# Performance work log

Measured on AMD Instinct MI355X. Metric: run time of the kernel, lower is better.

Reference implementation:

```python
import jax, jax.numpy as jnp
import numpy as np

N = 100000
E = 3200000
T = 8
F = 64


def _temporal_conv(x, src, dst, time_index, W, b):
    # time-bucketed segmented scatter-add: segment id = dst*T + t
    seg = dst * T + time_index                      # [E]
    msgs = x[src]                                   # [E, F] gather (x_j)
    agg = jax.ops.segment_sum(msgs, seg, num_segments=N * T)  # [N*T, F]
    cat = agg.reshape(N, T * x.shape[-1])           # concat over t blocks: [N, T*F]
    return jax.nn.relu(cat @ W + b)                 # temporal_lin + relu


def setup_inputs() -> dict:
    key = jax.random.key(0)
    ks = jax.random.split(key, 10)
    x = jax.random.normal(ks[0], (N, F), dtype=jnp.float32)
    edge_index = jax.random.randint(ks[1], (2, E), 0, N, dtype=jnp.int64)
    time_index = jax.random.randint(ks[2], (E,), 0, T, dtype=jnp.int64)
    s1 = 1.0 / np.sqrt(F * T)
    W1 = jax.random.uniform(ks[3], (F * T, 64), jnp.float32, -s1, s1)
    b1 = jax.random.uniform(ks[4], (64,), jnp.float32, -s1, s1)
    s2 = 1.0 / np.sqrt(64 * T)
    W2 = jax.random.uniform(ks[5], (64 * T, 64), jnp.float32, -s2, s2)
    b2 = jax.random.uniform(ks[6], (64,), jnp.float32, -s2, s2)
    s3 = 1.0 / np.sqrt(64)
    Wssl = jax.random.uniform(ks[7], (64, F), jnp.float32, -s3, s3)
    bssl = jax.random.uniform(ks[8], (F,), jnp.float32, -s3, s3)
    return {"x": x, "edge_index": edge_index, "time_index": time_index,
            "W1": W1, "b1": b1, "W2": W2, "b2": b2, "Wssl": Wssl, "bssl": bssl}


def reference(x, edge_index, time_index, W1, b1, W2, b2, Wssl, bssl):
    src, dst = edge_index[0], edge_index[1]  # flow source_to_target
    h = _temporal_conv(x, src, dst, time_index, W1, b1)
    h = jax.nn.relu(h)                        # outer relu in TemporalSSTGNN.forward
    h = _temporal_conv(h, src, dst, time_index, W2, b2)
    ssl = h @ Wssl + bssl                     # self_supervised_linear
    return (h, ssl)
```

## Files before the change

kernel.cpp:

```cpp
#include <hip/hip_runtime.h>
#include <hip/hip_bf16.h>

#define N_NODES 100000
#define N_EDGES 3200000
#define NB 391
#define NBP 400
#define CAP 9216
#define PCAP 20480
#define ZNODE N_NODES
#define NTILES 6250
#define AROW 520

typedef __attribute__((ext_vector_type(8))) short short8;
typedef __attribute__((ext_vector_type(4))) float floatx4;

__device__ __forceinline__ float bf2f(unsigned short u) {
    unsigned int x = ((unsigned int)u) << 16;
    return __builtin_bit_cast(float, x);
}
__device__ __forceinline__ unsigned short f2bf(float f) {
    unsigned int u = __builtin_bit_cast(unsigned int, f);
    unsigned int r = (u + 0x7FFFu + ((u >> 16) & 1u)) >> 16;
    return (unsigned short)r;
}


__global__ __launch_bounds__(1024) void k_bscatter(const int* __restrict__ ei,
                                                   const int* __restrict__ ti,
                                                   int* __restrict__ cursor,
                                                   unsigned int* __restrict__ words) {
    __shared__ int h[NBP];
    __shared__ int bb[NBP];
    int tid = threadIdx.x;
    if (tid < NBP) h[tid] = 0;
    __syncthreads();
    int base = blockIdx.x * 4096;
    int breg[4], ofs[4];
    unsigned wreg[4];
#pragma unroll
    for (int i = 0; i < 4; ++i) {
        int e = base + i * 1024 + tid;
        bool v = e < N_EDGES;
        int dst = v ? ei[N_EDGES + e] : 0;
        int src = v ? ei[e] : 0;
        int tt  = v ? ti[e] : 0;
        int b = dst >> 8;
        breg[i] = v ? b : -1;
        wreg[i] = ((unsigned)src << 11) | ((unsigned)(dst & 255) << 3) | (unsigned)tt;
        ofs[i] = v ? atomicAdd(&h[b], 1) : 0;
    }
    __syncthreads();
    if (tid < NB) {
        int c = h[tid];
        bb[tid] = c ? atomicAdd(&cursor[tid], c) : 0;
    }
    __syncthreads();
#pragma unroll
    for (int i = 0; i < 4; ++i)
        if (breg[i] >= 0) {
            int b = breg[i];
            words[b * CAP + bb[b] + ofs[i]] = wreg[i];
        }
}

__global__ __launch_bounds__(1024) void k_lsort(const int* __restrict__ cursor,
                                                const unsigned int* __restrict__ words,
                                                int2* __restrict__ node_pm,
                                                int* __restrict__ gid_pad) {
    __shared__ int h[2048];
    __shared__ int ps[1024];
    __shared__ int nb[256];
    __shared__ int s_ml[256];
    int tid = threadIdx.x;
    int b = blockIdx.x;
    int rb = b * CAP, re = rb + cursor[b];
    h[tid] = 0; h[tid + 1024] = 0;
    __syncthreads();
    unsigned wreg[9];
    int ofs[9];
#pragma unroll
    for (int i = 0; i < 9; ++i) {
        int e = rb + i * 1024 + tid;
        bool v = e < re;
        unsigned w = v ? words[e] : 0u;
        wreg[i] = w;
        ofs[i] = v ? atomicAdd(&h[w & 2047u], 1) : -1;
    }
    __syncthreads();
    int sz = 0;
    if (tid < 256) {
        int m = 0;
#pragma unroll
        for (int t = 0; t < 8; ++t) { int c = h[tid * 8 + t]; m = c > m ? c : m; }
        m = (m + 3) & ~3;
        if (m < 8) m = 8;
        s_ml[tid] = m;
        sz = m * 8;
    }
    ps[tid] = sz;
    __syncthreads();
    for (int off = 1; off < 1024; off <<= 1) {
        int t = (tid >= off) ? ps[tid - off] : 0;
        __syncthreads();
        ps[tid] += t;
        __syncthreads();
    }
    if (tid < 256) nb[tid] = ps[tid] - sz;
    __syncthreads();
    int bsz = ps[1023];
    int pbase = b * PCAP;
    for (int s = tid; s < bsz; s += 1024) gid_pad[pbase + s] = ZNODE;
    int gn = b * 256 + tid;
    if (tid < 256 && gn < N_NODES) node_pm[gn] = (int2){pbase + nb[tid], s_ml[tid]};
    __syncthreads();
#pragma unroll
    for (int i = 0; i < 9; ++i)
        if (ofs[i] >= 0) {
            unsigned w = wreg[i];
            int ls = (int)(w & 2047u);
            int nd = ls >> 3, t = ls & 7;
            gid_pad[pbase + nb[nd] + t * s_ml[nd] + ofs[i]] = (int)(w >> 11);
        }
}


__global__ void k_cvt(const float* __restrict__ x, unsigned short* __restrict__ xb,
                      unsigned short* __restrict__ h1b,
                      const float* __restrict__ W1, const float* __restrict__ W2,
                      const float* __restrict__ Wssl,
                      unsigned short* __restrict__ Wf1, unsigned short* __restrict__ Wf2,
                      unsigned short* __restrict__ Wsf) {
    int i = blockIdx.x * 256 + threadIdx.x;
    if (i < N_NODES * 64) xb[i] = f2bf(x[i]);
    if (i < 64) {
        xb[(size_t)ZNODE * 64 + i] = 0;
        h1b[(size_t)ZNODE * 64 + i] = 0;
    }
    if (i < 512 * 64) {
        int k = i >> 6, o = i & 63;
        int c = o >> 4, m = o & 15;
        int ks = k >> 5, q = (k >> 3) & 3, j = k & 7;
        int pos = (((c * 16 + ks) * 64) + (m + 16 * q)) * 8 + j;
        Wf1[pos] = f2bf(W1[i]);
        Wf2[pos] = f2bf(W2[i]);
    }
    if (i < 64 * 64) {
        int k = i >> 6, o = i & 63;
        int c = o >> 4, m = o & 15;
        int ks = k >> 5, q = (k >> 3) & 3, j = k & 7;
        int pos = (((c * 2 + ks) * 64) + (m + 16 * q)) * 8 + j;
        Wsf[pos] = f2bf(Wssl[i]);
    }
}


__device__ __forceinline__ void accum8(float* a, uint4 p) {
    a[0] += __builtin_bit_cast(float, p.x << 16);
    a[1] += __builtin_bit_cast(float, p.x & 0xFFFF0000u);
    a[2] += __builtin_bit_cast(float, p.y << 16);
    a[3] += __builtin_bit_cast(float, p.y & 0xFFFF0000u);
    a[4] += __builtin_bit_cast(float, p.z << 16);
    a[5] += __builtin_bit_cast(float, p.z & 0xFFFF0000u);
    a[6] += __builtin_bit_cast(float, p.w << 16);
    a[7] += __builtin_bit_cast(float, p.w & 0xFFFF0000u);
}

__global__ __launch_bounds__(512) void k_fused(const int2* __restrict__ node_pm,
                                               const int* __restrict__ gid_pad,
                                               const unsigned short* __restrict__ xb,
                                               const unsigned short* __restrict__ Wf,
                                               const float* __restrict__ bias,
                                               unsigned short* __restrict__ out_bf,
                                               float* __restrict__ out_f32) {
    __shared__ __align__(16) unsigned short Atile[32 * AROW];
    int tid = threadIdx.x;
    int wave = tid >> 6, lane = tid & 63;
    int node_base = blockIdx.x * 32;
    int tl = lane >> 3, fo = lane & 7;
    const uint4* xs = (const uint4*)xb;

    int2 pm[4];
#pragma unroll
    for (int i = 0; i < 4; ++i) pm[i] = node_pm[node_base + wave * 4 + i];

#pragma unroll
    for (int i = 0; i < 4; ++i) {
        int nl = wave * 4 + i;
        int pb = __builtin_amdgcn_readfirstlane(pm[i].x);
        int ml = __builtin_amdgcn_readfirstlane(pm[i].y);
        const int* gp = gid_pad + pb + tl * ml;
        float acc[8] = {0.f, 0.f, 0.f, 0.f, 0.f, 0.f, 0.f, 0.f};
        int k = 0;
#pragma unroll 1
        for (; k + 8 <= ml; k += 8) {
            int4 ga = *(const int4*)(gp + k);
            int4 gb = *(const int4*)(gp + k + 4);
            uint4 p0 = xs[((unsigned)ga.x << 3) + fo];
            uint4 p1 = xs[((unsigned)ga.y << 3) + fo];
            uint4 p2 = xs[((unsigned)ga.z << 3) + fo];
            uint4 p3 = xs[((unsigned)ga.w << 3) + fo];
            uint4 p4 = xs[((unsigned)gb.x << 3) + fo];
            uint4 p5 = xs[((unsigned)gb.y << 3) + fo];
            uint4 p6 = xs[((unsigned)gb.z << 3) + fo];
            uint4 p7 = xs[((unsigned)gb.w << 3) + fo];
            accum8(acc, p0); accum8(acc, p1); accum8(acc, p2); accum8(acc, p3);
            accum8(acc, p4); accum8(acc, p5); accum8(acc, p6); accum8(acc, p7);
        }
        if (k < ml) {
            int4 ga = *(const int4*)(gp + k);
            uint4 p0 = xs[((unsigned)ga.x << 3) + fo];
            uint4 p1 = xs[((unsigned)ga.y << 3) + fo];
            uint4 p2 = xs[((unsigned)ga.z << 3) + fo];
            uint4 p3 = xs[((unsigned)ga.w << 3) + fo];
            accum8(acc, p0); accum8(acc, p1); accum8(acc, p2); accum8(acc, p3);
        }
        unsigned r0, r1, r2, r3;
        asm("v_cvt_pk_bf16_f32 %0, %1, %2" : "=v"(r0) : "v"(acc[0]), "v"(acc[1]));
        asm("v_cvt_pk_bf16_f32 %0, %1, %2" : "=v"(r1) : "v"(acc[2]), "v"(acc[3]));
        asm("v_cvt_pk_bf16_f32 %0, %1, %2" : "=v"(r2) : "v"(acc[4]), "v"(acc[5]));
        asm("v_cvt_pk_bf16_f32 %0, %1, %2" : "=v"(r3) : "v"(acc[6]), "v"(acc[7]));
        uint4 st;
        st.x = r0; st.y = r1; st.z = r2; st.w = r3;
        *(uint4*)(&Atile[nl * AROW + tl * 64 + fo * 8]) = st;
    }
    __syncthreads();

    int nt = wave >> 2, c = wave & 3;
    int m = lane & 15, q = lane >> 4;
    floatx4 acc = (floatx4){0.f, 0.f, 0.f, 0.f};
    const short8* wf8 = (const short8*)Wf;
    const unsigned short* abase = &Atile[(nt * 16 + m) * AROW + q * 8];
#pragma unroll
    for (int ks = 0; ks < 16; ++ks) {
        short8 a = *(const short8*)(abase + ks * 32);
        short8 b = wf8[(c * 16 + ks) * 64 + lane];
        acc = __builtin_amdgcn_mfma_f32_16x16x32_bf16(a, b, acc, 0, 0, 0);
    }
    float bb = bias[c * 16 + m];
    int node0 = node_base + nt * 16;
#pragma unroll
    for (int i = 0; i < 4; ++i) {
        float v = acc[i] + bb;
        v = v > 0.f ? v : 0.f;
        int node = node0 + q * 4 + i;
        size_t idx = (size_t)node * 64 + c * 16 + m;
        if (out_bf)  out_bf[idx] = f2bf(v);
        if (out_f32) out_f32[idx] = v;
    }
}


__global__ __launch_bounds__(256) void k_sslm(const unsigned short* __restrict__ h2b,
                                              const unsigned short* __restrict__ Wsf,
                                              const float* __restrict__ bssl,
                                              float* __restrict__ out) {
    int wave = threadIdx.x >> 6, lane = threadIdx.x & 63;
    int tile = blockIdx.x * 4 + wave;
    if (tile >= NTILES) return;
    int m = lane & 15, q = lane >> 4;
    const unsigned short* arow = h2b + ((size_t)(tile * 16 + m)) * 64 + q * 8;
    floatx4 acc[4];
    for (int c = 0; c < 4; ++c) acc[c] = (floatx4){0.f, 0.f, 0.f, 0.f};
    const short8* wf8 = (const short8*)Wsf;
#pragma unroll
    for (int ks = 0; ks < 2; ++ks) {
        short8 a = *(const short8*)(arow + ks * 32);
#pragma unroll
        for (int c = 0; c < 4; ++c) {
            short8 b = wf8[(c * 2 + ks) * 64 + lane];
            acc[c] = __builtin_amdgcn_mfma_f32_16x16x32_bf16(a, b, acc[c], 0, 0, 0);
        }
    }
    int node0 = tile * 16;
#pragma unroll
    for (int c = 0; c < 4; ++c) {
        float bb = bssl[c * 16 + m];
#pragma unroll
        for (int i = 0; i < 4; ++i) {
            int node = node0 + q * 4 + i;
            out[(size_t)node * 64 + c * 16 + m] = acc[c][i] + bb;
        }
    }
}


extern "C" void kernel_launch(void* const* d_in, const int* in_sizes, int n_in,
                              void* d_out, int out_size, void* d_ws, size_t ws_size,
                              hipStream_t stream) {
    const float* x    = (const float*)d_in[0];
    const int*   ei   = (const int*)d_in[1];
    const int*   ti   = (const int*)d_in[2];
    const float* W1   = (const float*)d_in[3];
    const float* b1   = (const float*)d_in[4];
    const float* W2   = (const float*)d_in[5];
    const float* b2   = (const float*)d_in[6];
    const float* Wssl = (const float*)d_in[7];
    const float* bssl = (const float*)d_in[8];
    float* out = (float*)d_out;

    char* w = (char*)d_ws;
    auto alloc = [&](size_t bytes) -> char* {
        char* p = w;
        w += (bytes + 255) & ~(size_t)255;
        return p;
    };
    int* cursor   = (int*)alloc((size_t)NBP * 4);
    unsigned int* words = (unsigned int*)alloc((size_t)NB * CAP * 4);
    int2* node_pm = (int2*)alloc((size_t)N_NODES * 8);
    int* gid_pad  = (int*)alloc((size_t)NB * PCAP * 4);
    unsigned short* xb  = (unsigned short*)alloc((size_t)(N_NODES + 1) * 64 * 2);
    unsigned short* h1b = (unsigned short*)alloc((size_t)(N_NODES + 1) * 64 * 2);
    unsigned short* h2b = (unsigned short*)alloc((size_t)N_NODES * 64 * 2);
    unsigned short* Wf1 = (unsigned short*)alloc((size_t)512 * 64 * 2);
    unsigned short* Wf2 = (unsigned short*)alloc((size_t)512 * 64 * 2);
    unsigned short* Wsf = (unsigned short*)alloc((size_t)64 * 64 * 2);

    hipMemsetAsync(cursor, 0, (size_t)NBP * 4, stream);
    k_bscatter<<<(N_EDGES + 4095) / 4096, 1024, 0, stream>>>(ei, ti, cursor, words);
    k_lsort<<<NB, 1024, 0, stream>>>(cursor, words, node_pm, gid_pad);
    k_cvt<<<(N_NODES * 64 + 255) / 256, 256, 0, stream>>>(x, xb, h1b, W1, W2, Wssl,
                                                          Wf1, Wf2, Wsf);

    k_fused<<<N_NODES / 32, 512, 0, stream>>>(node_pm, gid_pad, xb, Wf1, b1, h1b, nullptr);
    k_fused<<<N_NODES / 32, 512, 0, stream>>>(node_pm, gid_pad, h1b, Wf2, b2, h2b, out);

    k_sslm<<<(NTILES + 3) / 4, 256, 0, stream>>>(h2b, Wsf, bssl, out + (size_t)N_NODES * 64);
}
```

Before: 323.7 us.

## Fuse conversion into scatter, SSL linear into second conv, restructure gather loop

Folds the bf16 conversion of x and the weights into the bucket-scatter kernel, with a vectorized packed convert, which drops one launch. Fuses the self-supervised 64x64 linear into the second fused conv kernel through shared memory, removing the h2 bf16 round trip and the k_sslm launch. The local sort prefix scan is replaced by wave shuffles. The gather loop now prefetches index lists for all four nodes and processes nodes in pairs with packed float2 accumulation to raise memory-level parallelism. The risks are higher register pressure in the fused kernel and a longer serialized tail in the scatter kernel.

```diff
diff --git a/kernel.cpp b/kernel.cpp
--- a/kernel.cpp
+++ b/kernel.cpp
@@ -8,27 +8,32 @@
 #define CAP 9216
 #define PCAP 20480
 #define ZNODE N_NODES
-#define NTILES 6250
 #define AROW 520
+#define HROW 72
 
 typedef __attribute__((ext_vector_type(8))) short short8;
 typedef __attribute__((ext_vector_type(4))) float floatx4;
-
-__device__ __forceinline__ float bf2f(unsigned short u) {
-    unsigned int x = ((unsigned int)u) << 16;
-    return __builtin_bit_cast(float, x);
-}
+typedef __attribute__((ext_vector_type(2))) float f32x2;
+
 __device__ __forceinline__ unsigned short f2bf(float f) {
     unsigned int u = __builtin_bit_cast(unsigned int, f);
     unsigned int r = (u + 0x7FFFu + ((u >> 16) & 1u)) >> 16;
     return (unsigned short)r;
 }
 
-
 __global__ __launch_bounds__(1024) void k_bscatter(const int* __restrict__ ei,
                                                    const int* __restrict__ ti,
                                                    int* __restrict__ cursor,
-                                                   unsigned int* __restrict__ words) {
+                                                   unsigned int* __restrict__ words,
+                                                   const float* __restrict__ x,
+                                                   unsigned short* __restrict__ xb,
+                                                   unsigned short* __restrict__ h1b,
+                                                   const float* __restrict__ W1,
+                                                   const float* __restrict__ W2,
+                                                   const float* __restrict__ Wssl,
+                                                   unsigned short* __restrict__ Wf1,
+                                                   unsigned short* __restrict__ Wf2,
+                                                   unsigned short* __restrict__ Wsf) {
     __shared__ int h[NBP];
     __shared__ int bb[NBP];
     int tid = threadIdx.x;
@@ -61,6 +66,39 @@
             int b = breg[i];
             words[b * CAP + bb[b] + ofs[i]] = wreg[i];
         }
+
+    int gtid = blockIdx.x * 1024 + tid;
+    size_t xo = (size_t)gtid * 8;
+    if (xo < (size_t)N_NODES * 64) {
+        float4 f0 = *(const float4*)(x + xo);
+        float4 f1 = *(const float4*)(x + xo + 4);
+        unsigned r0, r1, r2, r3;
+        asm("v_cvt_pk_bf16_f32 %0, %1, %2" : "=v"(r0) : "v"(f0.x), "v"(f0.y));
+        asm("v_cvt_pk_bf16_f32 %0, %1, %2" : "=v"(r1) : "v"(f0.z), "v"(f0.w));
+        asm("v_cvt_pk_bf16_f32 %0, %1, %2" : "=v"(r2) : "v"(f1.x), "v"(f1.y));
+        asm("v_cvt_pk_bf16_f32 %0, %1, %2" : "=v"(r3) : "v"(f1.z), "v"(f1.w));
+        uint4 st; st.x = r0; st.y = r1; st.z = r2; st.w = r3;
+        *(uint4*)(xb + xo) = st;
+    }
+    if (gtid < 64) {
+        xb[(size_t)ZNODE * 64 + gtid] = 0;
+        h1b[(size_t)ZNODE * 64 + gtid] = 0;
+    }
+    if (gtid < 512 * 64) {
+        int k = gtid >> 6, o = gtid & 63;
+        int c = o >> 4, m = o & 15;
+        int ks = k >> 5, q = (k >> 3) & 3, j = k & 7;
+        int pos = (((c * 16 + ks) * 64) + (m + 16 * q)) * 8 + j;
+        Wf1[pos] = f2bf(W1[gtid]);
+        Wf2[pos] = f2bf(W2[gtid]);
+    }
+    if (gtid < 64 * 64) {
+        int k = gtid >> 6, o = gtid & 63;
+        int c = o >> 4, m = o & 15;
+        int ks = k >> 5, q = (k >> 3) & 3, j = k & 7;
+        int pos = (((c * 2 + ks) * 64) + (m + 16 * q)) * 8 + j;
+        Wsf[pos] = f2bf(Wssl[gtid]);
+    }
 }
 
 __global__ __launch_bounds__(1024) void k_lsort(const int* __restrict__ cursor,
@@ -68,9 +106,9 @@
                                                 int2* __restrict__ node_pm,
                                                 int* __restrict__ gid_pad) {
     __shared__ int h[2048];
-    __shared__ int ps[1024];
     __shared__ int nb[256];
     __shared__ int s_ml[256];
+    __shared__ int wsum[4];
     int tid = threadIdx.x;
     int b = blockIdx.x;
     int rb = b * CAP, re = rb + cursor[b];
@@ -97,17 +135,21 @@
         s_ml[tid] = m;
         sz = m * 8;
     }
-    ps[tid] = sz;
-    __syncthreads();
-    for (int off = 1; off < 1024; off <<= 1) {
-        int t = (tid >= off) ? ps[tid - off] : 0;
-        __syncthreads();
-        ps[tid] += t;
-        __syncthreads();
-    }
-    if (tid < 256) nb[tid] = ps[tid] - sz;
-    __syncthreads();
-    int bsz = ps[1023];
+    int lane = tid & 63, wv = tid >> 6;
+    int inc = sz;
+#pragma unroll
+    for (int off = 1; off < 64; off <<= 1) {
+        int t = __shfl_up(inc, off, 64);
+        if (lane >= off) inc += t;
+    }
+    if (tid < 256 && lane == 63) wsum[wv] = inc;
+    __syncthreads();
+    int bsz = wsum[0] + wsum[1] + wsum[2] + wsum[3];
+    if (tid < 256) {
+        int basec = 0;
+        for (int w = 0; w < wv; ++w) basec += wsum[w];
+        nb[tid] = basec + inc - sz;
+    }
     int pbase = b * PCAP;
     for (int s = tid; s < bsz; s += 1024) gid_pad[pbase + s] = ZNODE;
     int gn = b * 256 + tid;
@@ -124,45 +166,16 @@
 }
 
 
-__global__ void k_cvt(const float* __restrict__ x, unsigned short* __restrict__ xb,
-                      unsigned short* __restrict__ h1b,
-                      const float* __restrict__ W1, const float* __restrict__ W2,
-                      const float* __restrict__ Wssl,
-                      unsigned short* __restrict__ Wf1, unsigned short* __restrict__ Wf2,
-                      unsigned short* __restrict__ Wsf) {
-    int i = blockIdx.x * 256 + threadIdx.x;
-    if (i < N_NODES * 64) xb[i] = f2bf(x[i]);
-    if (i < 64) {
-        xb[(size_t)ZNODE * 64 + i] = 0;
-        h1b[(size_t)ZNODE * 64 + i] = 0;
-    }
-    if (i < 512 * 64) {
-        int k = i >> 6, o = i & 63;
-        int c = o >> 4, m = o & 15;
-        int ks = k >> 5, q = (k >> 3) & 3, j = k & 7;
-        int pos = (((c * 16 + ks) * 64) + (m + 16 * q)) * 8 + j;
-        Wf1[pos] = f2bf(W1[i]);
-        Wf2[pos] = f2bf(W2[i]);
-    }
-    if (i < 64 * 64) {
-        int k = i >> 6, o = i & 63;
-        int c = o >> 4, m = o & 15;
-        int ks = k >> 5, q = (k >> 3) & 3, j = k & 7;
-        int pos = (((c * 2 + ks) * 64) + (m + 16 * q)) * 8 + j;
-        Wsf[pos] = f2bf(Wssl[i]);
-    }
-}
-
-
-__device__ __forceinline__ void accum8(float* a, uint4 p) {
-    a[0] += __builtin_bit_cast(float, p.x << 16);
-    a[1] += __builtin_bit_cast(float, p.x & 0xFFFF0000u);
-    a[2] += __builtin_bit_cast(float, p.y << 16);
-    a[3] += __builtin_bit_cast(float, p.y & 0xFFFF0000u);
-    a[4] += __builtin_bit_cast(float, p.z << 16);
-    a[5] += __builtin_bit_cast(float, p.z & 0xFFFF0000u);
-    a[6] += __builtin_bit_cast(float, p.w << 16);
-    a[7] += __builtin_bit_cast(float, p.w & 0xFFFF0000u);
+__device__ __forceinline__ void accumP(f32x2* a, uint4 p) {
+    uint2 u;
+    u.x = p.x << 16; u.y = p.x & 0xFFFF0000u;
+    a[0] += __builtin_bit_cast(f32x2, u);
+    u.x = p.y << 16; u.y = p.y & 0xFFFF0000u;
+    a[1] += __builtin_bit_cast(f32x2, u);
+    u.x = p.z << 16; u.y = p.z & 0xFFFF0000u;
+    a[2] += __builtin_bit_cast(f32x2, u);
+    u.x = p.w << 16; u.y = p.w & 0xFFFF0000u;
+    a[3] += __builtin_bit_cast(f32x2, u);
 }
 
 __global__ __launch_bounds__(512) void k_fused(const int2* __restrict__ node_pm,
@@ -170,8 +183,11 @@
                                                const unsigned short* __restrict__ xb,
                                                const unsigned short* __restrict__ Wf,
                                                const float* __restrict__ bias,
+                                               const unsigned short* __restrict__ Wsf,
+                                               const float* __restrict__ bssl,
                                                unsigned short* __restrict__ out_bf,
-                                               float* __restrict__ out_f32) {
+                                               float* __restrict__ out_f32,
+                                               float* __restrict__ ssl_out) {
     __shared__ __align__(16) unsigned short Atile[32 * AROW];
     int tid = threadIdx.x;
     int wave = tid >> 6, lane = tid & 63;
@@ -183,45 +199,77 @@
 #pragma unroll
     for (int i = 0; i < 4; ++i) pm[i] = node_pm[node_base + wave * 4 + i];
 
+    int pb[4], ml[4];
+    const int* gp[4];
 #pragma unroll
     for (int i = 0; i < 4; ++i) {
-        int nl = wave * 4 + i;
-        int pb = __builtin_amdgcn_readfirstlane(pm[i].x);
-        int ml = __builtin_amdgcn_readfirstlane(pm[i].y);
-        const int* gp = gid_pad + pb + tl * ml;
-        float acc[8] = {0.f, 0.f, 0.f, 0.f, 0.f, 0.f, 0.f, 0.f};
-        int k = 0;
+        pb[i] = __builtin_amdgcn_readfirstlane(pm[i].x);
+        ml[i] = __builtin_amdgcn_readfirstlane(pm[i].y);
+        gp[i] = gid_pad + pb[i] + tl * ml[i];
+    }
+    int4 ga[4], gb[4];
+#pragma unroll
+    for (int i = 0; i < 4; ++i) {
+        ga[i] = *(const int4*)(gp[i]);
+        gb[i] = *(const int4*)(gp[i] + 4);
+    }
+
+#pragma unroll
+    for (int pr = 0; pr < 2; ++pr) {
+        int i0 = pr * 2, i1 = i0 + 1;
+        uint4 p0 = xs[((unsigned)ga[i0].x << 3) + fo];
+        uint4 p1 = xs[((unsigned)ga[i0].y << 3) + fo];
+        uint4 p2 = xs[((unsigned)ga[i0].z << 3) + fo];
+        uint4 p3 = xs[((unsigned)ga[i0].w << 3) + fo];
+        uint4 p4 = xs[((unsigned)gb[i0].x << 3) + fo];
+        uint4 p5 = xs[((unsigned)gb[i0].y << 3) + fo];
+        uint4 p6 = xs[((unsigned)gb[i0].z << 3) + fo];
+        uint4 p7 = xs[((unsigned)gb[i0].w << 3) + fo];
+        uint4 q0 = xs[((unsigned)ga[i1].x << 3) + fo];
+        uint4 q1 = xs[((unsigned)ga[i1].y << 3) + fo];
+        uint4 q2 = xs[((unsigned)ga[i1].z << 3) + fo];
+        uint4 q3 = xs[((unsigned)ga[i1].w << 3) + fo];
+        uint4 q4 = xs[((unsigned)gb[i1].x << 3) + fo];
+        uint4 q5 = xs[((unsigned)gb[i1].y << 3) + fo];
+        uint4 q6 = xs[((unsigned)gb[i1].z << 3) + fo];
+        uint4 q7 = xs[((unsigned)gb[i1].w << 3) + fo];
+        f32x2 a0[4] = {{0.f,0.f},{0.f,0.f},{0.f,0.f},{0.f,0.f}};
+        f32x2 a1[4] = {{0.f,0.f},{0.f,0.f},{0.f,0.f},{0.f,0.f}};
+        accumP(a0, p0); accumP(a0, p1); accumP(a0, p2); accumP(a0, p3);
+        accumP(a0, p4); accumP(a0, p5); accumP(a0, p6); accumP(a0, p7);
+        accumP(a1, q0); accumP(a1, q1); accumP(a1, q2); accumP(a1, q3);
+        accumP(a1, q4); accumP(a1, q5); accumP(a1, q6); accumP(a1, q7);
 #pragma unroll 1
-        for (; k + 8 <= ml; k += 8) {
-            int4 ga = *(const int4*)(gp + k);
-            int4 gb = *(const int4*)(gp + k + 4);
-            uint4 p0 = xs[((unsigned)ga.x << 3) + fo];
-            uint4 p1 = xs[((unsigned)ga.y << 3) + fo];
-            uint4 p2 = xs[((unsigned)ga.z << 3) + fo];
-            uint4 p3 = xs[((unsigned)ga.w << 3) + fo];
-            uint4 p4 = xs[((unsigned)gb.x << 3) + fo];
-            uint4 p5 = xs[((unsigned)gb.y << 3) + fo];
-            uint4 p6 = xs[((unsigned)gb.z << 3) + fo];
-            uint4 p7 = xs[((unsigned)gb.w << 3) + fo];
-            accum8(acc, p0); accum8(acc, p1); accum8(acc, p2); accum8(acc, p3);
-            accum8(acc, p4); accum8(acc, p5); accum8(acc, p6); accum8(acc, p7);
-        }
-        if (k < ml) {
-            int4 ga = *(const int4*)(gp + k);
-            uint4 p0 = xs[((unsigned)ga.x << 3) + fo];
-            uint4 p1 = xs[((unsigned)ga.y << 3) + fo];
-            uint4 p2 = xs[((unsigned)ga.z << 3) + fo];
-            uint4 p3 = xs[((unsigned)ga.w << 3) + fo];
-            accum8(acc, p0); accum8(acc, p1); accum8(acc, p2); accum8(acc, p3);
+        for (int k = 8; k < ml[i0]; k += 4) {
+            int4 g = *(const int4*)(gp[i0] + k);
+            uint4 t0 = xs[((unsigned)g.x << 3) + fo];
+            uint4 t1 = xs[((unsigned)g.y << 3) + fo];
+            uint4 t2 = xs[((unsigned)g.z << 3) + fo];
+            uint4 t3 = xs[((unsigned)g.w << 3) + fo];
+            accumP(a0, t0); accumP(a0, t1); accumP(a0, t2); accumP(a0, t3);
+        }
+#pragma unroll 1
+        for (int k = 8; k < ml[i1]; k += 4) {
+            int4 g = *(const int4*)(gp[i1] + k);
+            uint4 t0 = xs[((unsigned)g.x << 3) + fo];
+            uint4 t1 = xs[((unsigned)g.y << 3) + fo];
+            uint4 t2 = xs[((unsigned)g.z << 3) + fo];
+            uint4 t3 = xs[((unsigned)g.w << 3) + fo];
+            accumP(a1, t0); accumP(a1, t1); accumP(a1, t2); accumP(a1, t3);
         }
         unsigned r0, r1, r2, r3;
-        asm("v_cvt_pk_bf16_f32 %0, %1, %2" : "=v"(r0) : "v"(acc[0]), "v"(acc[1]));
-        asm("v_cvt_pk_bf16_f32 %0, %1, %2" : "=v"(r1) : "v"(acc[2]), "v"(acc[3]));
-        asm("v_cvt_pk_bf16_f32 %0, %1, %2" : "=v"(r2) : "v"(acc[4]), "v"(acc[5]));
-        asm("v_cvt_pk_bf16_f32 %0, %1, %2" : "=v"(r3) : "v"(acc[6]), "v"(acc[7]));
-        uint4 st;
+        asm("v_cvt_pk_bf16_f32 %0, %1, %2" : "=v"(r0) : "v"(a0[0].x), "v"(a0[0].y));
+        asm("v_cvt_pk_bf16_f32 %0, %1, %2" : "=v"(r1) : "v"(a0[1].x), "v"(a0[1].y));
+        asm("v_cvt_pk_bf16_f32 %0, %1, %2" : "=v"(r2) : "v"(a0[2].x), "v"(a0[2].y));
+        asm("v_cvt_pk_bf16_f32 %0, %1, %2" : "=v"(r3) : "v"(a0[3].x), "v"(a0[3].y));
+        uint4 st; st.x = r0; st.y = r1; st.z = r2; st.w = r3;
+        *(uint4*)(&Atile[(wave * 4 + i0) * AROW + tl * 64 + fo * 8]) = st;
+        asm("v_cvt_pk_bf16_f32 %0, %1, %2" : "=v"(r0) : "v"(a1[0].x), "v"(a1[0].y));
+        asm("v_cvt_pk_bf16_f32 %0, %1, %2" : "=v"(r1) : "v"(a1[1].x), "v"(a1[1].y));
+        asm("v_cvt_pk_bf16_f32 %0, %1, %2" : "=v"(r2) : "v"(a1[2].x), "v"(a1[2].y));
+        asm("v_cvt_pk_bf16_f32 %0, %1, %2" : "=v"(r3) : "v"(a1[3].x), "v"(a1[3].y));
         st.x = r0; st.y = r1; st.z = r2; st.w = r3;
-        *(uint4*)(&Atile[nl * AROW + tl * 64 + fo * 8]) = st;
+        *(uint4*)(&Atile[(wave * 4 + i1) * AROW + tl * 64 + fo * 8]) = st;
     }
     __syncthreads();
 
@@ -238,47 +286,42 @@
     }
     float bb = bias[c * 16 + m];
     int node0 = node_base + nt * 16;
+    float vv[4];
 #pragma unroll
     for (int i = 0; i < 4; ++i) {
         float v = acc[i] + bb;
-        v = v > 0.f ? v : 0.f;
+        vv[i] = v > 0.f ? v : 0.f;
         int node = node0 + q * 4 + i;
         size_t idx = (size_t)node * 64 + c * 16 + m;
-        if (out_bf)  out_bf[idx] = f2bf(v);
-        if (out_f32) out_f32[idx] = v;
-    }
-}
-
-
-__global__ __launch_bounds__(256) void k_sslm(const unsigned short* __restrict__ h2b,
-                                              const unsigned short* __restrict__ Wsf,
-                                              const float* __restrict__ bssl,
-                                              float* __restrict__ out) {
-    int wave = threadIdx.x >> 6, lane = threadIdx.x & 63;
-    int tile = blockIdx.x * 4 + wave;
-    if (tile >= NTILES) return;
-    int m = lane & 15, q = lane >> 4;
-    const unsigned short* arow = h2b + ((size_t)(tile * 16 + m)) * 64 + q * 8;
-    floatx4 acc[4];
-    for (int c = 0; c < 4; ++c) acc[c] = (floatx4){0.f, 0.f, 0.f, 0.f};
-    const short8* wf8 = (const short8*)Wsf;
-#pragma unroll
-    for (int ks = 0; ks < 2; ++ks) {
-        short8 a = *(const short8*)(arow + ks * 32);
-#pragma unroll
-        for (int c = 0; c < 4; ++c) {
-            short8 b = wf8[(c * 2 + ks) * 64 + lane];
-            acc[c] = __builtin_amdgcn_mfma_f32_16x16x32_bf16(a, b, acc[c], 0, 0, 0);
-        }
-    }
-    int node0 = tile * 16;
-#pragma unroll
-    for (int c = 0; c < 4; ++c) {
-        float bb = bssl[c * 16 + m];
+        if (out_bf)  out_bf[idx] = f2bf(vv[i]);
+        if (out_f32) out_f32[idx] = vv[i];
+    }
+
+    if (ssl_out) {
+        __syncthreads();
+        unsigned short* Ht = Atile;
 #pragma unroll
         for (int i = 0; i < 4; ++i) {
-            int node = node0 + q * 4 + i;
-            out[(size_t)node * 64 + c * 16 + m] = acc[c][i] + bb;
+            int nl = nt * 16 + q * 4 + i;
+            Ht[nl * HROW + c * 16 + m] = f2bf(vv[i]);
+        }
+        __syncthreads();
+        int nt2 = wave >> 2, c2 = wave & 3;
+        floatx4 sacc = (floatx4){0.f, 0.f, 0.f, 0.f};
+        const short8* sw8 = (const short8*)Wsf;
+        const unsigned short* sab = &Ht[(nt2 * 16 + m) * HROW + q * 8];
+#pragma unroll
+        for (int ks = 0; ks < 2; ++ks) {
+            short8 a = *(const short8*)(sab + ks * 32);
+            short8 b = sw8[(c2 * 2 + ks) * 64 + lane];
+            sacc = __builtin_amdgcn_mfma_f32_16x16x32_bf16(a, b, sacc, 0, 0, 0);
+        }
+        float sb = bssl[c2 * 16 + m];
+        int n0 = node_base + nt2 * 16;
+#pragma unroll
+        for (int i = 0; i < 4; ++i) {
+            int node = n0 + q * 4 + i;
+            ssl_out[(size_t)node * 64 + c2 * 16 + m] = sacc[i] + sb;
         }
     }
 }
@@ -310,19 +353,19 @@
     int* gid_pad  = (int*)alloc((size_t)NB * PCAP * 4);
     unsigned short* xb  = (unsigned short*)alloc((size_t)(N_NODES + 1) * 64 * 2);
     unsigned short* h1b = (unsigned short*)alloc((size_t)(N_NODES + 1) * 64 * 2);
-    unsigned short* h2b = (unsigned short*)alloc((size_t)N_NODES * 64 * 2);
     unsigned short* Wf1 = (unsigned short*)alloc((size_t)512 * 64 * 2);
     unsigned short* Wf2 = (unsigned short*)alloc((size_t)512 * 64 * 2);
     unsigned short* Wsf = (unsigned short*)alloc((size_t)64 * 64 * 2);
 
     hipMemsetAsync(cursor, 0, (size_t)NBP * 4, stream);
-    k_bscatter<<<(N_EDGES + 4095) / 4096, 1024, 0, stream>>>(ei, ti, cursor, words);
+    k_bscatter<<<(N_EDGES + 4095) / 4096, 1024, 0, stream>>>(ei, ti, cursor, words,
+                                                             x, xb, h1b, W1, W2, Wssl,
+                                                             Wf1, Wf2, Wsf);
     k_lsort<<<NB, 1024, 0, stream>>>(cursor, words, node_pm, gid_pad);
-    k_cvt<<<(N_NODES * 64 + 255) / 256, 256, 0, stream>>>(x, xb, h1b, W1, W2, Wssl,
-                                                          Wf1, Wf2, Wsf);
-
-    k_fused<<<N_NODES / 32, 512, 0, stream>>>(node_pm, gid_pad, xb, Wf1, b1, h1b, nullptr);
-    k_fused<<<N_NODES / 32, 512, 0, stream>>>(node_pm, gid_pad, h1b, Wf2, b2, h2b, out);
-
-    k_sslm<<<(NTILES + 3) / 4, 256, 0, stream>>>(h2b, Wsf, bssl, out + (size_t)N_NODES * 64);
-}
+
+    k_fused<<<N_NODES / 32, 512, 0, stream>>>(node_pm, gid_pad, xb, Wf1, b1,
+                                              nullptr, nullptr, h1b, nullptr, nullptr);
+    k_fused<<<N_NODES / 32, 512, 0, stream>>>(node_pm, gid_pad, h1b, Wf2, b2,
+                                              Wsf, bssl, nullptr, out,
+                                              out + (size_t)N_NODES * 64);
+}
```

Result: faster. 303.1 us (-6.4%).
